# Optimization experiments

Measured on AMD Instinct MI355X. Metric: run time of the kernel, lower is better.

## Reference

```python
import jax, jax.numpy as jnp
import numpy as np

V, D, H, T, L, M = 32000, 768, 12, 2048, 4, 64
HD = D // H
EPS = 1e-5


def _layer_norm(x, scale, bias):
    mu = x.mean(-1, keepdims=True)
    var = ((x - mu) ** 2).mean(-1, keepdims=True)
    return (x - mu) * jax.lax.rsqrt(var + EPS) * scale + bias


def setup_inputs() -> dict:
    key = jax.random.key(0)
    ks = jax.random.split(key, 12)
    f32 = jnp.float32
    inp = {
        "tokens": jax.random.randint(ks[0], (1, T), 0, V, dtype=jnp.int32),
        "emb": jax.random.normal(ks[1], (V, D), f32) * 0.05,
        "pos": jax.random.normal(ks[2], (T, D), f32) * 0.05,
        "mem": jax.random.normal(ks[3], (M, D), f32) * 0.05,
        "ln1_s": jnp.ones((L, D), f32),
        "ln1_b": jnp.zeros((L, D), f32),
        "wq": jax.random.normal(ks[4], (L, D, D), f32) * (D ** -0.5),
        "wk": jax.random.normal(ks[5], (L, D, D), f32) * (D ** -0.5),
        "wv": jax.random.normal(ks[6], (L, D, D), f32) * (D ** -0.5),
        "wo": jax.random.normal(ks[7], (L, D, D), f32) * (D ** -0.5),
        "ln2_s": jnp.ones((L, D), f32),
        "ln2_b": jnp.zeros((L, D), f32),
        "w1": jax.random.normal(ks[8], (L, 4 * D, D), f32) * (D ** -0.5),
        "b1": jnp.zeros((L, 4 * D), f32),
        "w2": jax.random.normal(ks[9], (L, D, 4 * D), f32) * ((4 * D) ** -0.5),
        "b2": jnp.zeros((L, D), f32),
        "lnm_s": jnp.ones((D,), f32),
        "lnm_b": jnp.zeros((D,), f32),
    }
    return inp


def reference(tokens, emb, pos, mem, ln1_s, ln1_b, wq, wk, wv, wo,
              ln2_s, ln2_b, w1, b1, w2, b2, lnm_s, lnm_b):
    B, Tt = tokens.shape
    x = emb[tokens] + pos[:Tt][None]                       # [B,T,D]
    x = jnp.concatenate([jnp.broadcast_to(mem, (B, M, D)), x], axis=1)  # [B,S,D]
    S = M + Tt
    causal = jnp.tril(jnp.ones((S, S), bool))              # [S,S]
    neg_inf = jnp.finfo(x.dtype).min
    scale = 1.0 / np.sqrt(HD)

    def block(h, p):
        l1s, l1b, Wq, Wk, Wv, Wo, l2s, l2b, W1, B1, W2, B2 = p
        n = _layer_norm(h, l1s, l1b)
        q = (n @ Wq.T).reshape(B, S, H, HD).transpose(0, 2, 1, 3)  # bhsd
        k = (n @ Wk.T).reshape(B, S, H, HD).transpose(0, 2, 1, 3)
        v = (n @ Wv.T).reshape(B, S, H, HD).transpose(0, 2, 1, 3)
        scores = jnp.einsum('bhqd,bhkd->bhqk', q, k) * scale
        scores = jnp.where(causal[None, None], scores, neg_inf)
        attn = jax.nn.softmax(scores, axis=-1)
        o = jnp.einsum('bhqk,bhkd->bhqd', attn, v)
        o = o.transpose(0, 2, 1, 3).reshape(B, S, D) @ Wo.T
        h = h + o
        n = _layer_norm(h, l2s, l2b)
        ff = jax.nn.gelu(n @ W1.T + B1, approximate=True) @ W2.T + B2
        return h + ff, None

    x, _ = jax.lax.scan(block, x, (ln1_s, ln1_b, wq, wk, wv, wo,
                                   ln2_s, ln2_b, w1, b1, w2, b2))
    x = _layer_norm(x, lnm_s, lnm_b)
    return x[:, -M:, :]
```

## Files before the change

kernel.cpp:

```cpp
#include <hip/hip_runtime.h>
#include <math.h>

#define S_TOT 2112
#define SPAD  2176
#define DMODEL 768
#define QKVLD 2304
#define NMEM 64
#define NHEAD 12
#define HDIM 64
#define NQT 33
#define CHUNK 9
#define NZ 4

typedef unsigned short ushort_t;
typedef __attribute__((ext_vector_type(8))) short short8;
typedef __attribute__((ext_vector_type(4))) float f32x4;

__device__ __forceinline__ ushort_t f2bf(float f) {
    unsigned int u = __builtin_bit_cast(unsigned int, f);
    u = (u + 0x7FFFu + ((u >> 16) & 1u)) >> 16;
    return (ushort_t)u;
}
__device__ __forceinline__ float bf2f(ushort_t u) {
    unsigned int x = ((unsigned int)u) << 16;
    return __builtin_bit_cast(float, x);
}

#define WAIT_LGKM() __builtin_amdgcn_s_waitcnt(0xC07F)
#define BAR()       __builtin_amdgcn_s_barrier()

__global__ __launch_bounds__(256) void cvt6_kernel(
    const float* __restrict__ wq, const float* __restrict__ wk,
    const float* __restrict__ wv, const float* __restrict__ wo,
    const float* __restrict__ w1, const float* __restrict__ w2,
    ushort_t* __restrict__ wqkv, ushort_t* __restrict__ wob,
    ushort_t* __restrict__ w1b, ushort_t* __restrict__ w2b)
{
    const int DDv = (DMODEL * DMODEL) / 4;
    const int DFv = (DMODEL * 4 * DMODEL) / 4;
    int i = blockIdx.x * 256 + threadIdx.x;
    const float* src;
    ushort_t* dst;
    if (i < 3 * DDv) {
        if (i < DDv)          { src = wq + (size_t)i * 4; }
        else if (i < 2 * DDv) { src = wk + (size_t)(i - DDv) * 4; }
        else                  { src = wv + (size_t)(i - 2 * DDv) * 4; }
        dst = wqkv + (size_t)i * 4;
    } else if (i < 4 * DDv) {
        src = wo + (size_t)(i - 3 * DDv) * 4;
        dst = wob + (size_t)(i - 3 * DDv) * 4;
    } else if (i < 4 * DDv + DFv) {
        src = w1 + (size_t)(i - 4 * DDv) * 4;
        dst = w1b + (size_t)(i - 4 * DDv) * 4;
    } else {
        src = w2 + (size_t)(i - 4 * DDv - DFv) * 4;
        dst = w2b + (size_t)(i - 4 * DDv - DFv) * 4;
    }
    float4 v = *(const float4*)src;
    ushort4 o;
    o.x = f2bf(v.x); o.y = f2bf(v.y); o.z = f2bf(v.z); o.w = f2bf(v.w);
    *(ushort4*)dst = o;
}

__global__ __launch_bounds__(256) void embed_kernel(
    const int* __restrict__ tokens, const float* __restrict__ emb,
    const float* __restrict__ pos, const float* __restrict__ mem,
    float* __restrict__ x)
{
    int s = blockIdx.x;
    int tid = threadIdx.x;
    float* xr = x + (size_t)s * DMODEL;
    if (s >= S_TOT) {
        for (int d = tid; d < DMODEL; d += 256) xr[d] = 0.0f;
    } else if (s < NMEM) {
        const float* mr = mem + (size_t)s * DMODEL;
        for (int d = tid; d < DMODEL; d += 256) xr[d] = mr[d];
    } else {
        int t = s - NMEM;
        int tok = tokens[t];
        const float* er = emb + (size_t)tok * DMODEL;
        const float* pr = pos + (size_t)t * DMODEL;
        for (int d = tid; d < DMODEL; d += 256) xr[d] = er[d] + pr[d];
    }
}

template <typename OUT>
__global__ __launch_bounds__(256) void ln_kernel(
    const float* __restrict__ X, const float* __restrict__ g,
    const float* __restrict__ b, OUT* __restrict__ Y)
{
    __shared__ float red[256];
    int row = blockIdx.x, tid = threadIdx.x;
    const float* xr = X + (size_t)row * DMODEL;
    float v0 = xr[tid], v1 = xr[tid + 256], v2 = xr[tid + 512];
    red[tid] = v0 + v1 + v2;
    __syncthreads();
    for (int s = 128; s > 0; s >>= 1) {
        if (tid < s) red[tid] += red[tid + s];
        __syncthreads();
    }
    float mu = red[0] * (1.0f / 768.0f);
    __syncthreads();
    float d0 = v0 - mu, d1 = v1 - mu, d2 = v2 - mu;
    red[tid] = d0 * d0 + d1 * d1 + d2 * d2;
    __syncthreads();
    for (int s = 128; s > 0; s >>= 1) {
        if (tid < s) red[tid] += red[tid + s];
        __syncthreads();
    }
    float inv = rsqrtf(red[0] * (1.0f / 768.0f) + 1e-5f);
    OUT* yr = Y + (size_t)row * DMODEL;
    float o0 = d0 * inv * g[tid]       + b[tid];
    float o1 = d1 * inv * g[tid + 256] + b[tid + 256];
    float o2 = d2 * inv * g[tid + 512] + b[tid + 512];
    if constexpr (sizeof(OUT) == 2) {
        yr[tid] = f2bf(o0); yr[tid + 256] = f2bf(o1); yr[tid + 512] = f2bf(o2);
    } else {
        yr[tid] = o0; yr[tid + 256] = o1; yr[tid + 512] = o2;
    }
}

__global__ __launch_bounds__(512) void gemm_mfma(
    const ushort_t* __restrict__ A, const ushort_t* __restrict__ B,
    const float* __restrict__ bias, const float* __restrict__ resid,
    void* __restrict__ Cp, int K, int ldc, int ncol0, int act, int c_bf16)
{
    __shared__ ushort_t As[2][4096];
    __shared__ ushort_t Bs[2][4096];
    int tid = threadIdx.x;
    int l = tid & 63, w = tid >> 6;
    int wr = w >> 1, wc = w & 1;

    int gx = gridDim.x;
    int nwg = gx * gridDim.y;
    int orig = blockIdx.x + gx * blockIdx.y;
    int q = nwg >> 3, r = nwg & 7;
    int xcd = orig & 7, loc = orig >> 3;
    int swz = (xcd < r ? xcd * (q + 1) : r * (q + 1) + (xcd - r) * q) + loc;
    int m0 = (swz / gx) * 128, n0 = (swz % gx) * 128;

    int kz = blockIdx.z;
    int nsplit = gridDim.z;
    int Kc = K / nsplit;
    bool split = (nsplit > 1);

    int row = tid >> 2, g = tid & 3;
    int swoff = row * 64 + ((g ^ ((row >> 1) & 3)) << 4);
    const ushort_t* Ap = A + (size_t)(m0 + row) * K + kz * Kc + g * 8;
    const ushort_t* Bp = B + (size_t)(n0 + row) * K + kz * Kc + g * 8;

    int kc = l >> 4, mr = l & 15;
    int aoff[2], boff[4];
#pragma unroll
    for (int i = 0; i < 2; ++i) {
        int rr = wr * 32 + i * 16 + mr;
        aoff[i] = rr * 64 + ((kc ^ ((rr >> 1) & 3)) << 4);
    }
#pragma unroll
    for (int j = 0; j < 4; ++j) {
        int rr = wc * 64 + j * 16 + mr;
        boff[j] = rr * 64 + ((kc ^ ((rr >> 1) & 3)) << 4);
    }

    f32x4 acc[2][4];
#pragma unroll
    for (int i = 0; i < 2; ++i)
#pragma unroll
        for (int j = 0; j < 4; ++j)
            acc[i][j] = (f32x4){0.f, 0.f, 0.f, 0.f};

    int nk = Kc >> 5;

    auto kstep = [&](int bi) {
        const char* bA = (const char*)As[bi];
        const char* bB = (const char*)Bs[bi];
        short8 af[2], bfr[4];
#pragma unroll
        for (int i = 0; i < 2; ++i) af[i]  = *(const short8*)(bA + aoff[i]);
#pragma unroll
        for (int j = 0; j < 4; ++j) bfr[j] = *(const short8*)(bB + boff[j]);
#pragma unroll
        for (int i = 0; i < 2; ++i)
#pragma unroll
            for (int j = 0; j < 4; ++j)
                acc[i][j] = __builtin_amdgcn_mfma_f32_16x16x32_bf16(af[i], bfr[j], acc[i][j], 0, 0, 0);
    };
    auto commit = [&](short8& sa, short8& sb, int bi, int t) {
        *(short8*)((char*)As[bi] + swoff) = sa;
        *(short8*)((char*)Bs[bi] + swoff) = sb;
        int ko = (t < nk ? t : nk - 1) << 5;
        sa = *(const short8*)(Ap + ko);
        sb = *(const short8*)(Bp + ko);
    };

    {
        short8 a0 = *(const short8*)Ap;
        short8 b0 = *(const short8*)Bp;
        *(short8*)((char*)As[0] + swoff) = a0;
        *(short8*)((char*)Bs[0] + swoff) = b0;
    }
    short8 s1a = *(const short8*)(Ap + 32),  s1b = *(const short8*)(Bp + 32);
    short8 s2a = *(const short8*)(Ap + 64),  s2b = *(const short8*)(Bp + 64);
    short8 s3a = *(const short8*)(Ap + 96),  s3b = *(const short8*)(Bp + 96);
    short8 s0a = *(const short8*)(Ap + 128), s0b = *(const short8*)(Bp + 128);
    WAIT_LGKM(); BAR();

    for (int k = 0; k < nk; k += 4) {
        kstep(0);
        if (k + 1 < nk) commit(s1a, s1b, 1, k + 5);
        WAIT_LGKM(); BAR();
        if (k + 1 < nk) {
            kstep(1);
            if (k + 2 < nk) commit(s2a, s2b, 0, k + 6);
            WAIT_LGKM(); BAR();
        }
        if (k + 2 < nk) {
            kstep(0);
            if (k + 3 < nk) commit(s3a, s3b, 1, k + 7);
            WAIT_LGKM(); BAR();
        }
        if (k + 3 < nk) {
            kstep(1);
            if (k + 4 < nk) commit(s0a, s0b, 0, k + 8);
            WAIT_LGKM(); BAR();
        }
    }

    int lq = l >> 4;
#pragma unroll
    for (int i = 0; i < 2; ++i) {
#pragma unroll
        for (int rr = 0; rr < 4; ++rr) {
            int m = m0 + wr * 32 + i * 16 + lq * 4 + rr;
#pragma unroll
            for (int j = 0; j < 4; ++j) {
                int n = n0 + wc * 64 + j * 16 + mr;
                float v = acc[i][j][rr];
                if (bias && (!split || kz == 0)) v += bias[n];
                if (act) {
                    float u = v;
                    float t = 0.7978845608028654f * (u + 0.044715f * u * u * u);
                    v = u / (1.0f + __expf(-2.0f * t));
                }
                size_t idx = (size_t)m * ldc + ncol0 + n;
                if (split) {
                    atomicAdd((float*)Cp + idx, v);
                } else {
                    if (resid) v += resid[idx];
                    if (c_bf16) ((ushort_t*)Cp)[idx] = f2bf(v);
                    else        ((float*)Cp)[idx] = v;
                }
            }
        }
    }
}

__global__ __launch_bounds__(256) void attn_mfma(
    const ushort_t* __restrict__ qkv, ushort_t* __restrict__ Opart,
    float* __restrict__ ml)
{
    __shared__ ushort_t Qs[64][72];
    __shared__ ushort_t Ks[2][64][72];
    __shared__ ushort_t Vt[2][64][72];
    __shared__ ushort_t Ps[64][72];

    int qt = blockIdx.x;
    int h  = blockIdx.y;
    int z  = blockIdx.z;
    int kt0 = z * CHUNK;
    if (kt0 > qt) return;
    int kt1 = min(kt0 + CHUNK, qt + 1);

    int tid = threadIdx.x;
    int w = tid >> 6, lane = tid & 63;
    int quad = lane >> 4, l16 = lane & 15;
    int sr = lane;
    int dg = w;

    const size_t TSTRIDE = (size_t)64 * QKVLD;

    {
        const ushort_t* qp = qkv + (size_t)(qt * 64 + sr) * QKVLD + h * HDIM + dg * 16;
        *(short8*)&Qs[sr][dg * 16]     = *(const short8*)qp;
        *(short8*)&Qs[sr][dg * 16 + 8] = *(const short8*)(qp + 8);
    }

    const ushort_t* kp = qkv + (size_t)(kt0 * 64 + sr) * QKVLD + DMODEL + h * HDIM + dg * 16;
    const ushort_t* vp = kp + DMODEL;
    short8 pk0 = *(const short8*)kp, pk1 = *(const short8*)(kp + 8);
    short8 pv0 = *(const short8*)vp, pv1 = *(const short8*)(vp + 8);
    kp += TSTRIDE; vp += TSTRIDE;

    *(short8*)&Ks[0][sr][dg * 16]     = pk0;
    *(short8*)&Ks[0][sr][dg * 16 + 8] = pk1;
#pragma unroll
    for (int j = 0; j < 8; ++j) Vt[0][dg * 16 + j][sr] = (ushort_t)pv0[j];
#pragma unroll
    for (int j = 0; j < 8; ++j) Vt[0][dg * 16 + 8 + j][sr] = (ushort_t)pv1[j];

    pk0 = *(const short8*)kp; pk1 = *(const short8*)(kp + 8);
    pv0 = *(const short8*)vp; pv1 = *(const short8*)(vp + 8);
    kp += TSTRIDE; vp += TSTRIDE;

    WAIT_LGKM(); BAR();

    short8 qf[2];
    qf[0] = *(const short8*)&Qs[w * 16 + l16][quad * 8];
    qf[1] = *(const short8*)&Qs[w * 16 + l16][32 + quad * 8];

    float mstate[4] = {-1e30f, -1e30f, -1e30f, -1e30f};
    float lstate[4] = {0.f, 0.f, 0.f, 0.f};
    f32x4 accO[4];
#pragma unroll
    for (int j = 0; j < 4; ++j) accO[j] = (f32x4){0.f, 0.f, 0.f, 0.f};

    for (int kt = kt0; kt < kt1; ++kt) {
        int cb = (kt - kt0) & 1;

        f32x4 sacc[4];
#pragma unroll
        for (int nt = 0; nt < 4; ++nt) {
            sacc[nt] = (f32x4){0.f, 0.f, 0.f, 0.f};
            short8 kf0 = *(const short8*)&Ks[cb][nt * 16 + l16][quad * 8];
            short8 kf1 = *(const short8*)&Ks[cb][nt * 16 + l16][32 + quad * 8];
            sacc[nt] = __builtin_amdgcn_mfma_f32_16x16x32_bf16(qf[0], kf0, sacc[nt], 0, 0, 0);
            sacc[nt] = __builtin_amdgcn_mfma_f32_16x16x32_bf16(qf[1], kf1, sacc[nt], 0, 0, 0);
        }

        if (kt + 1 < kt1) {
            int nb = cb ^ 1;
            *(short8*)&Ks[nb][sr][dg * 16]     = pk0;
            *(short8*)&Ks[nb][sr][dg * 16 + 8] = pk1;
#pragma unroll
            for (int j = 0; j < 8; ++j) Vt[nb][dg * 16 + j][sr] = (ushort_t)pv0[j];
#pragma unroll
            for (int j = 0; j < 8; ++j) Vt[nb][dg * 16 + 8 + j][sr] = (ushort_t)pv1[j];
            pk0 = *(const short8*)kp; pk1 = *(const short8*)(kp + 8);
            pv0 = *(const short8*)vp; pv1 = *(const short8*)(vp + 8);
            kp += TSTRIDE; vp += TSTRIDE;
        }

        bool diag = (kt == qt);
        float s[4][4], rmax[4];
#pragma unroll
        for (int r = 0; r < 4; ++r) rmax[r] = -1e30f;
#pragma unroll
        for (int nt = 0; nt < 4; ++nt)
#pragma unroll
            for (int r = 0; r < 4; ++r) {
                float v = sacc[nt][r] * 0.125f;
                if (diag && (nt * 16 + l16) > (w * 16 + quad * 4 + r)) v = -1e30f;
                s[nt][r] = v;
                rmax[r] = fmaxf(rmax[r], v);
            }
#pragma unroll
        for (int r = 0; r < 4; ++r) {
            rmax[r] = fmaxf(rmax[r], __shfl_xor(rmax[r], 1));
            rmax[r] = fmaxf(rmax[r], __shfl_xor(rmax[r], 2));
            rmax[r] = fmaxf(rmax[r], __shfl_xor(rmax[r], 4));
            rmax[r] = fmaxf(rmax[r], __shfl_xor(rmax[r], 8));
        }
        float alpha[4];
#pragma unroll
        for (int r = 0; r < 4; ++r) {
            float mnew = fmaxf(mstate[r], rmax[r]);
            alpha[r] = __expf(mstate[r] - mnew);
            mstate[r] = mnew;
        }
        float rsum[4] = {0.f, 0.f, 0.f, 0.f};
#pragma unroll
        for (int nt = 0; nt < 4; ++nt)
#pragma unroll
            for (int r = 0; r < 4; ++r) {
                float p = __expf(s[nt][r] - mstate[r]);
                Ps[w * 16 + quad * 4 + r][nt * 16 + l16] = f2bf(p);
                rsum[r] += p;
            }
#pragma unroll
        for (int r = 0; r < 4; ++r) {
            rsum[r] += __shfl_xor(rsum[r], 1);
            rsum[r] += __shfl_xor(rsum[r], 2);
            rsum[r] += __shfl_xor(rsum[r], 4);
            rsum[r] += __shfl_xor(rsum[r], 8);
            lstate[r] = lstate[r] * alpha[r] + rsum[r];
        }
#pragma unroll
        for (int j = 0; j < 4; ++j)
#pragma unroll
            for (int r = 0; r < 4; ++r) accO[j][r] *= alpha[r];

        short8 pf0 = *(const short8*)&Ps[w * 16 + l16][quad * 8];
        short8 pf1 = *(const short8*)&Ps[w * 16 + l16][32 + quad * 8];
#pragma unroll
        for (int j = 0; j < 4; ++j) {
            short8 vf0 = *(const short8*)&Vt[cb][j * 16 + l16][quad * 8];
            short8 vf1 = *(const short8*)&Vt[cb][j * 16 + l16][32 + quad * 8];
            accO[j] = __builtin_amdgcn_mfma_f32_16x16x32_bf16(pf0, vf0, accO[j], 0, 0, 0);
            accO[j] = __builtin_amdgcn_mfma_f32_16x16x32_bf16(pf1, vf1, accO[j], 0, 0, 0);
        }

        WAIT_LGKM(); BAR();
    }

    size_t pidx = (size_t)(h * NQT + qt) * NZ + z;
#pragma unroll
    for (int j = 0; j < 4; ++j)
#pragma unroll
        for (int r = 0; r < 4; ++r) {
            int row = w * 16 + quad * 4 + r;
            Opart[pidx * 4096 + row * 64 + j * 16 + l16] = f2bf(accO[j][r]);
        }
    if (l16 == 0) {
        float* mlr = ml + pidx * 128;
#pragma unroll
        for (int r = 0; r < 4; ++r) {
            int row = w * 16 + quad * 4 + r;
            mlr[row * 2]     = mstate[r];
            mlr[row * 2 + 1] = lstate[r];
        }
    }
}

__global__ __launch_bounds__(256) void attn_combine(
    const ushort_t* __restrict__ Opart, const float* __restrict__ ml,
    ushort_t* __restrict__ att)
{
    int qt = blockIdx.x, h = blockIdx.y;
    int nch = (qt + CHUNK) / CHUNK;
    int t = threadIdx.x;
    int row = t >> 2, c0 = (t & 3) << 4;
    size_t pb = (size_t)(h * NQT + qt) * NZ;

    float mv[NZ], lv[NZ];
    float M = -1e30f;
#pragma unroll
    for (int z = 0; z < NZ; ++z) {
        mv[z] = -1e30f; lv[z] = 0.f;
        if (z < nch) {
            const float* p = ml + (pb + z) * 128 + row * 2;
            mv[z] = p[0]; lv[z] = p[1];
            M = fmaxf(M, mv[z]);
        }
    }
    float denom = 0.f;
    float sc[NZ];
#pragma unroll
    for (int z = 0; z < NZ; ++z) {
        sc[z] = 0.f;
        if (z < nch) { sc[z] = __expf(mv[z] - M); denom += sc[z] * lv[z]; }
    }
    float inv = 1.0f / denom;

    float o[16];
#pragma unroll
    for (int i = 0; i < 16; ++i) o[i] = 0.f;
#pragma unroll
    for (int z = 0; z < NZ; ++z) {
        if (z < nch) {
            const ushort_t* op = Opart + (pb + z) * 4096 + row * 64 + c0;
            short8 a0 = *(const short8*)op;
            short8 a1 = *(const short8*)(op + 8);
#pragma unroll
            for (int i = 0; i < 8; ++i) o[i]     += sc[z] * bf2f((ushort_t)a0[i]);
#pragma unroll
            for (int i = 0; i < 8; ++i) o[i + 8] += sc[z] * bf2f((ushort_t)a1[i]);
        }
    }
    ushort_t* dst = att + (size_t)(qt * 64 + row) * DMODEL + h * HDIM + c0;
    short8 r0, r1;
#pragma unroll
    for (int i = 0; i < 8; ++i) {
        r0[i] = (short)f2bf(o[i] * inv);
        r1[i] = (short)f2bf(o[i + 8] * inv);
    }
    *(short8*)dst = r0;
    *(short8*)(dst + 8) = r1;
}

extern "C" void kernel_launch(void* const* d_in, const int* in_sizes, int n_in,
                              void* d_out, int out_size, void* d_ws, size_t ws_size,
                              hipStream_t stream) {
    const int*   tokens = (const int*)d_in[0];
    const float* emb    = (const float*)d_in[1];
    const float* pos    = (const float*)d_in[2];
    const float* mem    = (const float*)d_in[3];
    const float* ln1_s  = (const float*)d_in[4];
    const float* ln1_b  = (const float*)d_in[5];
    const float* wq     = (const float*)d_in[6];
    const float* wk     = (const float*)d_in[7];
    const float* wv     = (const float*)d_in[8];
    const float* wo     = (const float*)d_in[9];
    const float* ln2_s  = (const float*)d_in[10];
    const float* ln2_b  = (const float*)d_in[11];
    const float* w1     = (const float*)d_in[12];
    const float* b1     = (const float*)d_in[13];
    const float* w2     = (const float*)d_in[14];
    const float* b2     = (const float*)d_in[15];
    const float* lnm_s  = (const float*)d_in[16];
    const float* lnm_b  = (const float*)d_in[17];
    float* out = (float*)d_out;

    const int D = DMODEL, L = 4, FF = 4 * DMODEL, SP = SPAD;
    const int DD = D * D;
    const int DF = D * FF;

    float*    x    = (float*)d_ws;
    ushort_t* qkvb = (ushort_t*)(x + (size_t)SP * D);
    ushort_t* nbuf = qkvb + (size_t)SP * 3 * D;
    ushort_t* attb = nbuf + (size_t)SP * D;
    ushort_t* ffh  = attb + (size_t)SP * D;
    ushort_t* wqkv = ffh  + (size_t)SP * FF;
    ushort_t* wob  = wqkv + (size_t)3 * DD;
    ushort_t* w1b  = wob  + (size_t)DD;
    ushort_t* w2b  = w1b  + (size_t)DF;
    ushort_t* Opart = ffh;
    float*    mlbuf = (float*)nbuf;

    embed_kernel<<<SP, 256, 0, stream>>>(tokens, emb, pos, mem, x);

    dim3 gQKV(18, 17);
    dim3 gO(6, 17, 4);
    dim3 gF1(24, 17);
    dim3 gF2(6, 17, 4);
    dim3 gA(NQT, NHEAD, NZ);
    dim3 gC(NQT, NHEAD);
    const int cvtBlocks = (4 * DD + 2 * DF) / 1024;

    for (int l = 0; l < L; ++l) {
        cvt6_kernel<<<cvtBlocks, 256, 0, stream>>>(
            wq + (size_t)l * DD, wk + (size_t)l * DD, wv + (size_t)l * DD,
            wo + (size_t)l * DD, w1 + (size_t)l * DF, w2 + (size_t)l * DF,
            wqkv, wob, w1b, w2b);

        ln_kernel<ushort_t><<<SP, 256, 0, stream>>>(x, ln1_s + l * D, ln1_b + l * D, nbuf);
        gemm_mfma<<<gQKV, 512, 0, stream>>>(nbuf, wqkv, nullptr, nullptr,
                                            qkvb, D, 3 * D, 0, 0, 1);
        attn_mfma<<<gA, 256, 0, stream>>>(qkvb, Opart, mlbuf);
        attn_combine<<<gC, 256, 0, stream>>>(Opart, mlbuf, attb);
        gemm_mfma<<<gO, 512, 0, stream>>>(attb, wob, nullptr, nullptr,
                                          x, D, D, 0, 0, 0);
        ln_kernel<ushort_t><<<SP, 256, 0, stream>>>(x, ln2_s + l * D, ln2_b + l * D, nbuf);
        gemm_mfma<<<gF1, 512, 0, stream>>>(nbuf, w1b, b1 + (size_t)l * FF, nullptr,
                                           ffh, D, FF, 0, 1, 1);
        gemm_mfma<<<gF2, 512, 0, stream>>>(ffh, w2b, b2 + (size_t)l * D, nullptr,
                                           x, FF, D, 0, 0, 0);
    }
    ln_kernel<float><<<NMEM, 256, 0, stream>>>(x + (size_t)(S_TOT - NMEM) * D,
                                               lnm_s, lnm_b, out);
}
```

Baseline: 917.8 us.

## Double GEMM K-tile to 64 and convert all layer weights in one launch

```diff
diff --git a/kernel.cpp b/kernel.cpp
--- a/kernel.cpp
+++ b/kernel.cpp
@@ -29,33 +29,33 @@
 #define WAIT_LGKM() __builtin_amdgcn_s_waitcnt(0xC07F)
 #define BAR()       __builtin_amdgcn_s_barrier()
 
-__global__ __launch_bounds__(256) void cvt6_kernel(
+__global__ __launch_bounds__(256) void cvt_all_kernel(
     const float* __restrict__ wq, const float* __restrict__ wk,
     const float* __restrict__ wv, const float* __restrict__ wo,
     const float* __restrict__ w1, const float* __restrict__ w2,
-    ushort_t* __restrict__ wqkv, ushort_t* __restrict__ wob,
-    ushort_t* __restrict__ w1b, ushort_t* __restrict__ w2b)
+    ushort_t* __restrict__ wAll)
 {
-    const int DDv = (DMODEL * DMODEL) / 4;
-    const int DFv = (DMODEL * 4 * DMODEL) / 4;
+    const int DD = DMODEL * DMODEL;
+    const int DF = DMODEL * 4 * DMODEL;
+    const int DDv = DD / 4;
+    const int DFv = DF / 4;
+    const int PERLv = 4 * DDv + 2 * DFv;
     int i = blockIdx.x * 256 + threadIdx.x;
+    int layer = i / PERLv;
+    int r = i - layer * PERLv;
     const float* src;
-    ushort_t* dst;
-    if (i < 3 * DDv) {
-        if (i < DDv)          { src = wq + (size_t)i * 4; }
-        else if (i < 2 * DDv) { src = wk + (size_t)(i - DDv) * 4; }
-        else                  { src = wv + (size_t)(i - 2 * DDv) * 4; }
-        dst = wqkv + (size_t)i * 4;
-    } else if (i < 4 * DDv) {
-        src = wo + (size_t)(i - 3 * DDv) * 4;
-        dst = wob + (size_t)(i - 3 * DDv) * 4;
-    } else if (i < 4 * DDv + DFv) {
-        src = w1 + (size_t)(i - 4 * DDv) * 4;
-        dst = w1b + (size_t)(i - 4 * DDv) * 4;
+    if (r < 3 * DDv) {
+        if (r < DDv)          src = wq + (size_t)layer * DD + (size_t)r * 4;
+        else if (r < 2 * DDv) src = wk + (size_t)layer * DD + (size_t)(r - DDv) * 4;
+        else                  src = wv + (size_t)layer * DD + (size_t)(r - 2 * DDv) * 4;
+    } else if (r < 4 * DDv) {
+        src = wo + (size_t)layer * DD + (size_t)(r - 3 * DDv) * 4;
+    } else if (r < 4 * DDv + DFv) {
+        src = w1 + (size_t)layer * DF + (size_t)(r - 4 * DDv) * 4;
     } else {
-        src = w2 + (size_t)(i - 4 * DDv - DFv) * 4;
-        dst = w2b + (size_t)(i - 4 * DDv - DFv) * 4;
-    }
+        src = w2 + (size_t)layer * DF + (size_t)(r - 4 * DDv - DFv) * 4;
+    }
+    ushort_t* dst = wAll + (size_t)layer * PERLv * 4 + (size_t)r * 4;
     float4 v = *(const float4*)src;
     ushort4 o;
     o.x = f2bf(v.x); o.y = f2bf(v.y); o.z = f2bf(v.z); o.w = f2bf(v.w);
@@ -125,8 +125,8 @@
     const float* __restrict__ bias, const float* __restrict__ resid,
     void* __restrict__ Cp, int K, int ldc, int ncol0, int act, int c_bf16)
 {
-    __shared__ ushort_t As[2][4096];
-    __shared__ ushort_t Bs[2][4096];
+    __shared__ ushort_t As[2][8192];
+    __shared__ ushort_t Bs[2][8192];
     int tid = threadIdx.x;
     int l = tid & 63, w = tid >> 6;
     int wr = w >> 1, wc = w & 1;
@@ -145,21 +145,27 @@
     bool split = (nsplit > 1);
 
     int row = tid >> 2, g = tid & 3;
-    int swoff = row * 64 + ((g ^ ((row >> 1) & 3)) << 4);
-    const ushort_t* Ap = A + (size_t)(m0 + row) * K + kz * Kc + g * 8;
-    const ushort_t* Bp = B + (size_t)(n0 + row) * K + kz * Kc + g * 8;
+    int sw0 = row * 128 + (((g)     ^ (row & 7)) << 4);
+    int sw1 = row * 128 + (((g + 4) ^ (row & 7)) << 4);
+    const ushort_t* Ap = A + (size_t)(m0 + row) * K + kz * Kc;
+    const ushort_t* Bp = B + (size_t)(n0 + row) * K + kz * Kc;
+    int go0 = g * 8, go1 = (g + 4) * 8;
 
     int kc = l >> 4, mr = l & 15;
-    int aoff[2], boff[4];
+    int aoff[2][2], boff[4][2];
 #pragma unroll
     for (int i = 0; i < 2; ++i) {
         int rr = wr * 32 + i * 16 + mr;
-        aoff[i] = rr * 64 + ((kc ^ ((rr >> 1) & 3)) << 4);
+#pragma unroll
+        for (int kh = 0; kh < 2; ++kh)
+            aoff[i][kh] = rr * 128 + (((kc + 4 * kh) ^ (rr & 7)) << 4);
     }
 #pragma unroll
     for (int j = 0; j < 4; ++j) {
         int rr = wc * 64 + j * 16 + mr;
-        boff[j] = rr * 64 + ((kc ^ ((rr >> 1) & 3)) << 4);
+#pragma unroll
+        for (int kh = 0; kh < 2; ++kh)
+            boff[j][kh] = rr * 128 + (((kc + 4 * kh) ^ (rr & 7)) << 4);
     }
 
     f32x4 acc[2][4];
@@ -169,59 +175,65 @@
         for (int j = 0; j < 4; ++j)
             acc[i][j] = (f32x4){0.f, 0.f, 0.f, 0.f};
 
-    int nk = Kc >> 5;
+    int nk = Kc >> 6;
 
     auto kstep = [&](int bi) {
         const char* bA = (const char*)As[bi];
         const char* bB = (const char*)Bs[bi];
-        short8 af[2], bfr[4];
-#pragma unroll
-        for (int i = 0; i < 2; ++i) af[i]  = *(const short8*)(bA + aoff[i]);
-#pragma unroll
-        for (int j = 0; j < 4; ++j) bfr[j] = *(const short8*)(bB + boff[j]);
+        short8 af[2][2], bfr[4][2];
 #pragma unroll
         for (int i = 0; i < 2; ++i)
 #pragma unroll
-            for (int j = 0; j < 4; ++j)
-                acc[i][j] = __builtin_amdgcn_mfma_f32_16x16x32_bf16(af[i], bfr[j], acc[i][j], 0, 0, 0);
+            for (int kh = 0; kh < 2; ++kh)
+                af[i][kh] = *(const short8*)(bA + aoff[i][kh]);
+#pragma unroll
+        for (int j = 0; j < 4; ++j)
+#pragma unroll
+            for (int kh = 0; kh < 2; ++kh)
+                bfr[j][kh] = *(const short8*)(bB + boff[j][kh]);
+#pragma unroll
+        for (int kh = 0; kh < 2; ++kh)
+#pragma unroll
+            for (int i = 0; i < 2; ++i)
+#pragma unroll
+                for (int j = 0; j < 4; ++j)
+                    acc[i][j] = __builtin_amdgcn_mfma_f32_16x16x32_bf16(af[i][kh], bfr[j][kh], acc[i][j], 0, 0, 0);
     };
-    auto commit = [&](short8& sa, short8& sb, int bi, int t) {
-        *(short8*)((char*)As[bi] + swoff) = sa;
-        *(short8*)((char*)Bs[bi] + swoff) = sb;
-        int ko = (t < nk ? t : nk - 1) << 5;
-        sa = *(const short8*)(Ap + ko);
-        sb = *(const short8*)(Bp + ko);
+    auto commit = [&](short8& a0, short8& a1, short8& b0, short8& b1, int bi, int t) {
+        *(short8*)((char*)As[bi] + sw0) = a0;
+        *(short8*)((char*)As[bi] + sw1) = a1;
+        *(short8*)((char*)Bs[bi] + sw0) = b0;
+        *(short8*)((char*)Bs[bi] + sw1) = b1;
+        int ko = (t < nk ? t : nk - 1) << 6;
+        a0 = *(const short8*)(Ap + ko + go0);
+        a1 = *(const short8*)(Ap + ko + go1);
+        b0 = *(const short8*)(Bp + ko + go0);
+        b1 = *(const short8*)(Bp + ko + go1);
     };
 
     {
-        short8 a0 = *(const short8*)Ap;
-        short8 b0 = *(const short8*)Bp;
-        *(short8*)((char*)As[0] + swoff) = a0;
-        *(short8*)((char*)Bs[0] + swoff) = b0;
-    }
-    short8 s1a = *(const short8*)(Ap + 32),  s1b = *(const short8*)(Bp + 32);
-    short8 s2a = *(const short8*)(Ap + 64),  s2b = *(const short8*)(Bp + 64);
-    short8 s3a = *(const short8*)(Ap + 96),  s3b = *(const short8*)(Bp + 96);
-    short8 s0a = *(const short8*)(Ap + 128), s0b = *(const short8*)(Bp + 128);
+        short8 a0 = *(const short8*)(Ap + go0);
+        short8 a1 = *(const short8*)(Ap + go1);
+        short8 b0 = *(const short8*)(Bp + go0);
+        short8 b1 = *(const short8*)(Bp + go1);
+        *(short8*)((char*)As[0] + sw0) = a0;
+        *(short8*)((char*)As[0] + sw1) = a1;
+        *(short8*)((char*)Bs[0] + sw0) = b0;
+        *(short8*)((char*)Bs[0] + sw1) = b1;
+    }
+    short8 oa0 = *(const short8*)(Ap + 64 + go0), oa1 = *(const short8*)(Ap + 64 + go1);
+    short8 ob0 = *(const short8*)(Bp + 64 + go0), ob1 = *(const short8*)(Bp + 64 + go1);
+    short8 ea0 = *(const short8*)(Ap + 128 + go0), ea1 = *(const short8*)(Ap + 128 + go1);
+    short8 eb0 = *(const short8*)(Bp + 128 + go0), eb1 = *(const short8*)(Bp + 128 + go1);
     WAIT_LGKM(); BAR();
 
-    for (int k = 0; k < nk; k += 4) {
+    for (int k = 0; k < nk; k += 2) {
         kstep(0);
-        if (k + 1 < nk) commit(s1a, s1b, 1, k + 5);
+        if (k + 1 < nk) commit(oa0, oa1, ob0, ob1, 1, k + 3);
         WAIT_LGKM(); BAR();
         if (k + 1 < nk) {
             kstep(1);
-            if (k + 2 < nk) commit(s2a, s2b, 0, k + 6);
-            WAIT_LGKM(); BAR();
-        }
-        if (k + 2 < nk) {
-            kstep(0);
-            if (k + 3 < nk) commit(s3a, s3b, 1, k + 7);
-            WAIT_LGKM(); BAR();
-        }
-        if (k + 3 < nk) {
-            kstep(1);
-            if (k + 4 < nk) commit(s0a, s0b, 0, k + 8);
+            if (k + 2 < nk) commit(ea0, ea1, eb0, eb1, 0, k + 4);
             WAIT_LGKM(); BAR();
         }
     }
@@ -503,20 +515,20 @@
     const int D = DMODEL, L = 4, FF = 4 * DMODEL, SP = SPAD;
     const int DD = D * D;
     const int DF = D * FF;
+    const size_t PERL = (size_t)4 * DD + 2 * DF;
 
     float*    x    = (float*)d_ws;
     ushort_t* qkvb = (ushort_t*)(x + (size_t)SP * D);
     ushort_t* nbuf = qkvb + (size_t)SP * 3 * D;
     ushort_t* attb = nbuf + (size_t)SP * D;
     ushort_t* ffh  = attb + (size_t)SP * D;
-    ushort_t* wqkv = ffh  + (size_t)SP * FF;
-    ushort_t* wob  = wqkv + (size_t)3 * DD;
-    ushort_t* w1b  = wob  + (size_t)DD;
-    ushort_t* w2b  = w1b  + (size_t)DF;
+    ushort_t* wAll = ffh  + (size_t)SP * FF;
     ushort_t* Opart = ffh;
     float*    mlbuf = (float*)nbuf;
 
     embed_kernel<<<SP, 256, 0, stream>>>(tokens, emb, pos, mem, x);
+    cvt_all_kernel<<<(4 * (4 * DD + 2 * DF)) / 1024, 256, 0, stream>>>(
+        wq, wk, wv, wo, w1, w2, wAll);
 
     dim3 gQKV(18, 17);
     dim3 gO(6, 17, 4);
@@ -524,13 +536,12 @@
     dim3 gF2(6, 17, 4);
     dim3 gA(NQT, NHEAD, NZ);
     dim3 gC(NQT, NHEAD);
-    const int cvtBlocks = (4 * DD + 2 * DF) / 1024;
 
     for (int l = 0; l < L; ++l) {
-        cvt6_kernel<<<cvtBlocks, 256, 0, stream>>>(
-            wq + (size_t)l * DD, wk + (size_t)l * DD, wv + (size_t)l * DD,
-            wo + (size_t)l * DD, w1 + (size_t)l * DF, w2 + (size_t)l * DF,
-            wqkv, wob, w1b, w2b);
+        ushort_t* wqkv = wAll + (size_t)l * PERL;
+        ushort_t* wob  = wqkv + (size_t)3 * DD;
+        ushort_t* w1b  = wob  + (size_t)DD;
+        ushort_t* w2b  = w1b  + (size_t)DF;
 
         ln_kernel<ushort_t><<<SP, 256, 0, stream>>>(x, ln1_s + l * D, ln1_b + l * D, nbuf);
         gemm_mfma<<<gQKV, 512, 0, stream>>>(nbuf, wqkv, nullptr, nullptr,
```

After: 883.5 us. 3.7% less time.
